# Kernel optimization log

Measured on AMD Instinct MI355X. Metric: run time of the kernel, lower is better.

The kernel has to match this reference:

```python
import jax, jax.numpy as jnp
import numpy as np

N_NODES = 100000
N_EDGES = 1600000
D_IN = 128
D_HID = 64
D_EMB = 64
EDGE_DIM = 2 * D_EMB  # 128
N_CASES = 4
BATCH = 16384
BN_EPS = 1e-5


def gcn_conv(x, src, dst, n, W, b):
    # PyG GCNConv: linear transform, add self-loops, sym-normalized aggregation
    h = x @ W  # [N, out]
    loop = jnp.arange(n, dtype=src.dtype)
    s = jnp.concatenate([src, loop])
    d = jnp.concatenate([dst, loop])
    deg = jax.ops.segment_sum(jnp.ones(s.shape[0], dtype=h.dtype), d, num_segments=n)
    dinv = jnp.where(deg > 0, deg ** -0.5, 0.0)
    norm = dinv[s] * dinv[d]  # [E+N]
    msg = h[s] * norm[:, None]
    return jax.ops.segment_sum(msg, d, num_segments=n) + b


def batchnorm(h, gamma, beta):
    # BatchNorm1d in training mode: biased batch statistics over nodes
    mu = h.mean(0)
    var = jnp.mean((h - mu) ** 2, axis=0)
    return (h - mu) * jax.lax.rsqrt(var + BN_EPS) * gamma + beta


def gcn_net(x, src, dst, n, W1, b1, g, be, W2, b2):
    h = gcn_conv(x, src, dst, n, W1, b1)
    h = jax.nn.relu(batchnorm(h, g, be))
    return gcn_conv(h, src, dst, n, W2, b2)


def setup_inputs() -> dict:
    key = jax.random.key(0)
    ks = jax.random.split(key, 20)
    inp = {
        "x": jax.random.normal(ks[0], (N_NODES, D_IN), dtype=jnp.float32),
        "edge_index": jax.random.randint(ks[1], (2, N_EDGES), 0, N_NODES, dtype=jnp.int32),
        "users_tensor": jax.random.randint(ks[2], (BATCH,), 0, 50000, dtype=jnp.int64) if jax.config.jax_enable_x64 else jax.random.randint(ks[2], (BATCH,), 0, 50000, dtype=jnp.int32),
        "items_tensor": jax.random.randint(ks[3], (BATCH,), 0, N_NODES, dtype=jnp.int32),
    }
    s = 0.05
    # generalized GCN params
    inp["W1g"] = jax.random.normal(ks[4], (D_IN, D_HID), dtype=jnp.float32) * s
    inp["b1g"] = jnp.zeros((D_HID,), jnp.float32)
    inp["g1g"] = jnp.ones((D_HID,), jnp.float32)
    inp["be1g"] = jnp.zeros((D_HID,), jnp.float32)
    inp["W2g"] = jax.random.normal(ks[5], (D_HID, D_EMB), dtype=jnp.float32) * s
    inp["b2g"] = jnp.zeros((D_EMB,), jnp.float32)
    # specific GCN params
    inp["W1s"] = jax.random.normal(ks[6], (D_IN, D_HID), dtype=jnp.float32) * s
    inp["b1s"] = jnp.zeros((D_HID,), jnp.float32)
    inp["g1s"] = jnp.ones((D_HID,), jnp.float32)
    inp["be1s"] = jnp.zeros((D_HID,), jnp.float32)
    inp["W2s"] = jax.random.normal(ks[7], (D_HID, D_EMB), dtype=jnp.float32) * s
    inp["b2s"] = jnp.zeros((D_EMB,), jnp.float32)
    # fusion gate (note: original forward uses hidden1 for BOTH inputs)
    inp["Wf1"] = jax.random.normal(ks[8], (EDGE_DIM, EDGE_DIM), dtype=jnp.float32) * s
    inp["Wsig"] = jax.random.normal(ks[9], (2 * EDGE_DIM, 1), dtype=jnp.float32) * s
    # heads
    inp["Wtc"] = jax.random.normal(ks[10], (EDGE_DIM, N_CASES), dtype=jnp.float32) * s
    inp["btc"] = jnp.zeros((N_CASES,), jnp.float32)
    inp["Wp"] = jax.random.normal(ks[11], (EDGE_DIM, 2), dtype=jnp.float32) * s
    inp["bp"] = jnp.zeros((2,), jnp.float32)
    return inp


def reference(x, edge_index, users_tensor, items_tensor,
              W1g, b1g, g1g, be1g, W2g, b2g,
              W1s, b1s, g1s, be1s, W2s, b2s,
              Wf1, Wsig, Wtc, btc, Wp, bp):
    n = x.shape[0]
    src, dst = edge_index[0], edge_index[1]

    nodes_gen = gcn_net(x, src, dst, n, W1g, b1g, g1g, be1g, W2g, b2g)  # [N, D_EMB]
    nodes_spec = gcn_net(x, src, dst, n, W1s, b1s, g1s, be1s, W2s, b2s)

    gen = jnp.concatenate([nodes_gen[users_tensor], nodes_gen[items_tensor]], axis=1)   # [B, 2E]
    spec = jnp.concatenate([nodes_spec[users_tensor], nodes_spec[items_tensor]], axis=1)

    h1 = jnp.tanh(gen @ Wf1)
    h2 = jnp.tanh(spec @ Wf1)  # original reuses hidden1
    z = jax.nn.sigmoid(jnp.concatenate([h1, h2], axis=1) @ Wsig)  # [B,1]
    fused = z * h1 + (1.0 - z) * h2

    link_output = fused @ Wp + bp
    generalized_output = gen @ Wtc + btc
    return (link_output, generalized_output)
```

## Files before the change

### kernel.cpp

```cpp
#include <hip/hip_runtime.h>
#include <hip/hip_bf16.h>


#define ELL_CAP 64
#define BCAP 8192
#define ACHUNK 5120

typedef __attribute__((ext_vector_type(8))) short short8v;
typedef __attribute__((ext_vector_type(4))) float f32x4;

static __device__ __forceinline__ float wred64(float v) {
#pragma unroll
  for (int m = 32; m; m >>= 1) v += __shfl_xor(v, m, 64);
  return v;
}

static __device__ __forceinline__ unsigned short f2bf(float f) {
  unsigned u = __float_as_uint(f);
  unsigned r = (u + 0x7fffu + ((u >> 16) & 1u)) >> 16;
  return (unsigned short)r;
}
static __device__ __forceinline__ unsigned packbf(float a, float b) {
  return (unsigned)f2bf(a) | ((unsigned)f2bf(b) << 16);
}
static __device__ __forceinline__ float bflo(unsigned u) {
  return __uint_as_float(u << 16);
}
static __device__ __forceinline__ float bfhi(unsigned u) {
  return __uint_as_float(u & 0xffff0000u);
}

__global__ void k_prep(const float* __restrict__ x, unsigned* __restrict__ bff,
                       int* __restrict__ gbump, float* __restrict__ stats,
                       const float* __restrict__ W1g, const float* __restrict__ b1g,
                       const float* __restrict__ W1s, const float* __restrict__ b1s,
                       const float* __restrict__ W2g, const float* __restrict__ b2g,
                       const float* __restrict__ W2s, const float* __restrict__ b2s,
                       const float* __restrict__ Wf1,
                       short* __restrict__ Wb1, short* __restrict__ Wb2,
                       short* __restrict__ WbH, float* __restrict__ bc1,
                       float* __restrict__ bc2, int n, int NB) {
  int idx = blockIdx.x * 256 + threadIdx.x;
  int n16 = n * 16;
  if (idx < n16) {
    const float4* f4 = (const float4*)x;
    float4 a = f4[idx * 2], b = f4[idx * 2 + 1];
    uint4 o;
    o.x = packbf(a.x, a.y);
    o.y = packbf(a.z, a.w);
    o.z = packbf(b.x, b.y);
    o.w = packbf(b.z, b.w);
    ((uint4*)bff)[idx] = o;
  }
  if (idx < 16384) {
    int k = idx >> 7, c = idx & 127;
    int pi = (k >> 3) * 1024 + c * 8 + (k & 7);
    float w1 = (c < 64) ? W1g[k * 64 + c] : W1s[k * 64 + (c - 64)];
    Wb1[pi] = (short)f2bf(w1);
    float w2 = 0.f;
    if (k < 64 && c < 64) w2 = W2g[k * 64 + c];
    else if (k >= 64 && c >= 64) w2 = W2s[(k - 64) * 64 + (c - 64)];
    Wb2[pi] = (short)f2bf(w2);
    WbH[pi] = (short)f2bf(Wf1[k * 128 + c]);
  }
  if (idx < 128) {
    bc1[idx] = (idx < 64) ? b1g[idx] : b1s[idx - 64];
    bc2[idx] = (idx < 64) ? b2g[idx] : b2s[idx - 64];
  }
  if (idx < NB) gbump[idx] = idx * BCAP;
  if (idx < 2048) stats[idx] = 0.f;
}

__global__ __launch_bounds__(256) void k_bucketA(
    const int* __restrict__ src, const int* __restrict__ dst,
    int* __restrict__ gbump, unsigned* __restrict__ ebuf, int E, int NB) {
  __shared__ int hist[512];
  __shared__ int gbase[512];
  int t = threadIdx.x;
  int e0 = blockIdx.x * ACHUNK;
  int m = min(ACHUNK, E - e0);
  for (int b = t; b < NB; b += 256) hist[b] = 0;
  __syncthreads();
  for (int i = t; i < m; i += 256) atomicAdd(&hist[dst[e0 + i] >> 8], 1);
  __syncthreads();
  for (int b = t; b < NB; b += 256) {
    gbase[b] = hist[b] ? atomicAdd(&gbump[b], hist[b]) : 0;
    hist[b] = 0;
  }
  __syncthreads();
  for (int i = t; i < m; i += 256) {
    int d = dst[e0 + i];
    int s = src[e0 + i];
    int b = d >> 8;
    int off = gbase[b] + atomicAdd(&hist[b], 1);
    if (off < (b + 1) * BCAP)
      ebuf[off] = ((unsigned)s << 8) | (unsigned)(d & 255);
  }
}

__global__ __launch_bounds__(256) void k_csrB(
    const unsigned* __restrict__ ebuf, const int* __restrict__ gbump,
    int* __restrict__ cnt, int* __restrict__ col, int n) {
  __shared__ int lbump[256];
  int b = blockIdx.x;
  lbump[threadIdx.x] = 0;
  __syncthreads();
  int base = b * BCAP;
  int m = min(gbump[b] - base, BCAP);
  for (int i = threadIdx.x; i < m; i += 256) {
    unsigned p = ebuf[base + i];
    int dloc = p & 255;
    int slot = atomicAdd(&lbump[dloc], 1);
    if (slot < ELL_CAP)
      col[(b * 256 + dloc) * ELL_CAP + slot] = (int)(p >> 8);
  }
  __syncthreads();
  int node = b * 256 + threadIdx.x;
  if (node < n) cnt[node] = lbump[threadIdx.x];
}

template <bool BN>
__global__ __launch_bounds__(256) void k_agg(
    const unsigned* __restrict__ featb, unsigned* __restrict__ outb,
    const int* __restrict__ cnt, const int* __restrict__ col,
    const float* __restrict__ stats, const float* __restrict__ g1g,
    const float* __restrict__ be1g, const float* __restrict__ g1s,
    const float* __restrict__ be1s, float inv_n, int n) {
  __shared__ float sc_sh[128], sf_sh[128];
  if (BN) {
    int c = threadIdx.x;
    if (c < 128) {
      float s = 0.f, q = 0.f;
#pragma unroll
      for (int k = 0; k < 8; k++) {
        s += stats[k * 256 + c];
        q += stats[k * 256 + 128 + c];
      }
      float mu = s * inv_n;
      float var = q * inv_n - mu * mu;
      float gam = (c < 64) ? g1g[c] : g1s[c - 64];
      float bet = (c < 64) ? be1g[c] : be1s[c - 64];
      float scv = gam * rsqrtf(var + 1e-5f);
      sc_sh[c] = scv;
      sf_sh[c] = bet - mu * scv;
    }
    __syncthreads();
  }
  int node = blockIdx.x * 16 + (threadIdx.x >> 4);
  if (node >= n) return;
  int t = threadIdx.x & 15;
  float sc[8], sf[8];
  if (BN) {
#pragma unroll
    for (int j = 0; j < 8; j++) {
      sc[j] = sc_sh[8 * t + j];
      sf[j] = sf_sh[8 * t + j];
    }
  }
  const uint4* f4 = (const uint4*)featb;
  int cn = cnt[node];
  float di = rsqrtf((float)(cn + 1));
  float acc[8];
  {
    uint4 sv = f4[(size_t)node * 16 + t];
    float f[8] = {bflo(sv.x), bfhi(sv.x), bflo(sv.y), bfhi(sv.y),
                  bflo(sv.z), bfhi(sv.z), bflo(sv.w), bfhi(sv.w)};
#pragma unroll
    for (int j = 0; j < 8; j++) {
      if (BN) f[j] = fmaxf(f[j] * sc[j] + sf[j], 0.f);
      acc[j] = f[j] * di;
    }
  }
  int m = min(cn, ELL_CAP);
  const int4* cl = (const int4*)&col[(size_t)node * ELL_CAP];
  int i = 0;
  for (; i + 4 <= m; i += 4) {
    int4 c4 = cl[i >> 2];
    int ss[4] = {c4.x, c4.y, c4.z, c4.w};
#pragma unroll
    for (int q = 0; q < 4; q++) {
      int s = ss[q];
      float w = rsqrtf((float)(cnt[s] + 1));
      uint4 v = f4[(size_t)s * 16 + t];
      float f[8] = {bflo(v.x), bfhi(v.x), bflo(v.y), bfhi(v.y),
                    bflo(v.z), bfhi(v.z), bflo(v.w), bfhi(v.w)};
#pragma unroll
      for (int j = 0; j < 8; j++) {
        if (BN) f[j] = fmaxf(f[j] * sc[j] + sf[j], 0.f);
        acc[j] += f[j] * w;
      }
    }
  }
  for (; i < m; ++i) {
    int s = col[(size_t)node * ELL_CAP + i];
    float w = rsqrtf((float)(cnt[s] + 1));
    uint4 v = f4[(size_t)s * 16 + t];
    float f[8] = {bflo(v.x), bfhi(v.x), bflo(v.y), bfhi(v.y),
                  bflo(v.z), bfhi(v.z), bflo(v.w), bfhi(v.w)};
#pragma unroll
    for (int j = 0; j < 8; j++) {
      if (BN) f[j] = fmaxf(f[j] * sc[j] + sf[j], 0.f);
      acc[j] += f[j] * w;
    }
  }
  uint4 o;
  o.x = packbf(acc[0] * di, acc[1] * di);
  o.y = packbf(acc[2] * di, acc[3] * di);
  o.z = packbf(acc[4] * di, acc[5] * di);
  o.w = packbf(acc[6] * di, acc[7] * di);
  ((uint4*)outb)[(size_t)node * 16 + t] = o;
}

template <bool CBF16, bool STATS, bool TANH, bool GATHER>
__global__ __launch_bounds__(256) void k_mgemm(
    const unsigned* __restrict__ Abf, const float* __restrict__ nodes,
    const int* __restrict__ users, const int* __restrict__ items,
    const short* __restrict__ Wb, const float* __restrict__ bias,
    void* __restrict__ Cvp, int M, float* __restrict__ stats) {
  __shared__ short Wl[16384];
  __shared__ float shs[128], shq[128];
  {
    const uint4* s4 = (const uint4*)Wb;
    uint4* d4 = (uint4*)Wl;
    for (int i = threadIdx.x; i < 2048; i += 256) d4[i] = s4[i];
  }
  if (STATS && threadIdx.x < 128) { shs[threadIdx.x] = 0.f; shq[threadIdx.x] = 0.f; }
  __syncthreads();
  int lane = threadIdx.x & 63;
  int wv = threadIdx.x >> 6;
  int l15 = lane & 15;
  int l4 = lane >> 4;
  int row = blockIdx.x * 64 + wv * 16 + l15;
  int rc = min(row, M - 1);
  bool valid = row < M;

  short8v afr[4];
  if (GATHER) {
    int fo = blockIdx.y * 64;
    const float* pu = nodes + (size_t)users[rc] * 128 + fo;
    const float* pi = nodes + (size_t)items[rc] * 128 + fo;
#pragma unroll
    for (int ks = 0; ks < 4; ks++) {
      int k = ks * 32 + l4 * 8;
      const float* p = (ks < 2) ? (pu + k) : (pi + (k - 64));
      float4 x0 = *(const float4*)p;
      float4 x1 = *(const float4*)(p + 4);
      union { short s[8]; short8v v; } u;
      u.s[0] = (short)f2bf(x0.x); u.s[1] = (short)f2bf(x0.y);
      u.s[2] = (short)f2bf(x0.z); u.s[3] = (short)f2bf(x0.w);
      u.s[4] = (short)f2bf(x1.x); u.s[5] = (short)f2bf(x1.y);
      u.s[6] = (short)f2bf(x1.z); u.s[7] = (short)f2bf(x1.w);
      afr[ks] = u.v;
    }
  } else {
    const short* Ab = (const short*)Abf + (size_t)rc * 128;
#pragma unroll
    for (int ks = 0; ks < 4; ks++)
      afr[ks] = *(const short8v*)(Ab + ks * 32 + l4 * 8);
  }

  f32x4 acc[8];
#pragma unroll
  for (int nt = 0; nt < 8; nt++) acc[nt] = (f32x4){0.f, 0.f, 0.f, 0.f};
#pragma unroll
  for (int nt = 0; nt < 8; nt++) {
#pragma unroll
    for (int ks = 0; ks < 4; ks++) {
      int kb = ks * 4 + l4;
      short8v w = *(const short8v*)&Wl[kb * 1024 + (nt * 16 + l15) * 8];
      acc[nt] = __builtin_amdgcn_mfma_f32_16x16x32_bf16(w, afr[ks], acc[nt], 0, 0, 0);
    }
  }

#pragma unroll
  for (int nt = 0; nt < 8; nt++) {
    int c0 = nt * 16 + l4 * 4;
    float o[4];
#pragma unroll
    for (int r = 0; r < 4; r++) o[r] = acc[nt][r];
    if (bias) {
      float4 bv = *(const float4*)(bias + c0);
      o[0] += bv.x; o[1] += bv.y; o[2] += bv.z; o[3] += bv.w;
    }
    if (TANH) {
#pragma unroll
      for (int r = 0; r < 4; r++) o[r] = tanhf(o[r]);
    }
    if (STATS) {
      float s[4], q[4];
#pragma unroll
      for (int r = 0; r < 4; r++) {
        s[r] = valid ? o[r] : 0.f;
        q[r] = s[r] * s[r];
      }
#pragma unroll
      for (int m = 1; m < 16; m <<= 1) {
#pragma unroll
        for (int r = 0; r < 4; r++) {
          s[r] += __shfl_xor(s[r], m, 64);
          q[r] += __shfl_xor(q[r], m, 64);
        }
      }
      if (l15 == 0) {
#pragma unroll
        for (int r = 0; r < 4; r++) {
          atomicAdd(&shs[c0 + r], s[r]);
          atomicAdd(&shq[c0 + r], q[r]);
        }
      }
    }
    if (valid) {
      if (CBF16) {
        unsigned* Cb = (unsigned*)Cvp;
        uint2 p;
        p.x = packbf(o[0], o[1]);
        p.y = packbf(o[2], o[3]);
        *(uint2*)&Cb[(size_t)row * 64 + (c0 >> 1)] = p;
      } else {
        float* Cf = (float*)Cvp + (size_t)blockIdx.y * M * 128;
        *(float4*)&Cf[(size_t)row * 128 + c0] = make_float4(o[0], o[1], o[2], o[3]);
      }
    }
  }
  if (STATS) {
    __syncthreads();
    if (threadIdx.x < 128) {
      float* st = stats + (blockIdx.x & 7) * 256;
      atomicAdd(&st[threadIdx.x], shs[threadIdx.x]);
      atomicAdd(&st[128 + threadIdx.x], shq[threadIdx.x]);
    }
  }
}

__global__ void k_head(const float* __restrict__ G1, const float* __restrict__ G2,
                       const float* __restrict__ nodes, const int* __restrict__ users,
                       const int* __restrict__ items, const float* __restrict__ Wsig,
                       const float* __restrict__ Wtc, const float* __restrict__ btc,
                       const float* __restrict__ Wp, const float* __restrict__ bp,
                       float* __restrict__ out, int B) {
  int l = threadIdx.x & 63;
  int wave = (blockIdx.x * 256 + threadIdx.x) >> 6;
  int nw = (gridDim.x * 256) >> 6;
  for (int b = wave; b < B; b += nw) {
    const float* g1 = G1 + (size_t)b * 128;
    const float* g2 = G2 + (size_t)b * 128;
    int u = users[b], it = items[b];
    float h1a = g1[l], h1b = g1[64 + l];
    float h2a = g2[l], h2b = g2[64 + l];
    float ga = nodes[(size_t)u * 128 + l];
    float gb = nodes[(size_t)it * 128 + l];
    float zp = h1a * Wsig[l] + h1b * Wsig[64 + l] + h2a * Wsig[128 + l] + h2b * Wsig[192 + l];
    float z = wred64(zp);
    z = 1.f / (1.f + expf(-z));
    float fa = z * h1a + (1.f - z) * h2a;
    float fb = z * h1b + (1.f - z) * h2b;
    float p0 = wred64(fa * Wp[l * 2] + fb * Wp[(64 + l) * 2]);
    float p1 = wred64(fa * Wp[l * 2 + 1] + fb * Wp[(64 + l) * 2 + 1]);
    float t0 = wred64(ga * Wtc[l * 4] + gb * Wtc[(64 + l) * 4]);
    float t1 = wred64(ga * Wtc[l * 4 + 1] + gb * Wtc[(64 + l) * 4 + 1]);
    float t2 = wred64(ga * Wtc[l * 4 + 2] + gb * Wtc[(64 + l) * 4 + 2]);
    float t3 = wred64(ga * Wtc[l * 4 + 3] + gb * Wtc[(64 + l) * 4 + 3]);
    if (l == 0) {
      out[b * 2] = p0 + bp[0];
      out[b * 2 + 1] = p1 + bp[1];
      float* go = out + 2 * B;
      go[b * 4] = t0 + btc[0];
      go[b * 4 + 1] = t1 + btc[1];
      go[b * 4 + 2] = t2 + btc[2];
      go[b * 4 + 3] = t3 + btc[3];
    }
  }
}

extern "C" void kernel_launch(void* const* d_in, const int* in_sizes, int n_in,
                              void* d_out, int out_size, void* d_ws, size_t ws_size,
                              hipStream_t stream) {
  const float* x = (const float*)d_in[0];
  const int* ei = (const int*)d_in[1];
  const int* users = (const int*)d_in[2];
  const int* items = (const int*)d_in[3];
  const float* W1g = (const float*)d_in[4];
  const float* b1g = (const float*)d_in[5];
  const float* g1g = (const float*)d_in[6];
  const float* be1g = (const float*)d_in[7];
  const float* W2g = (const float*)d_in[8];
  const float* b2g = (const float*)d_in[9];
  const float* W1s = (const float*)d_in[10];
  const float* b1s = (const float*)d_in[11];
  const float* g1s = (const float*)d_in[12];
  const float* be1s = (const float*)d_in[13];
  const float* W2s = (const float*)d_in[14];
  const float* b2s = (const float*)d_in[15];
  const float* Wf1 = (const float*)d_in[16];
  const float* Wsig = (const float*)d_in[17];
  const float* Wtc = (const float*)d_in[18];
  const float* btc = (const float*)d_in[19];
  const float* Wp = (const float*)d_in[20];
  const float* bp = (const float*)d_in[21];

  int n = in_sizes[0] / 128;
  int E = in_sizes[1] / 2;
  int B = in_sizes[2];
  int NB = (n + 255) >> 8;
  const int* srcp = ei;
  const int* dstp = ei + E;
  float* out = (float*)d_out;

  char* w = (char*)d_ws;
  auto alloc = [&](size_t bytes) -> char* {
    char* p = w;
    w += (bytes + 255) & ~(size_t)255;
    return p;
  };
  unsigned* xab = (unsigned*)alloc((size_t)n * 64 * 4);
  float* big1 = (float*)alloc((size_t)n * 128 * 4);
  unsigned* bff = (unsigned*)alloc((size_t)n * 128 * 2);
  int* col = (int*)alloc((size_t)n * ELL_CAP * 4);
  unsigned* ebuf = (unsigned*)alloc((size_t)NB * BCAP * 4);
  int* cnt = (int*)alloc((size_t)n * 4);
  int* gbump = (int*)alloc(512 * 4);
  short* Wb1 = (short*)alloc(16384 * 2);
  short* Wb2 = (short*)alloc(16384 * 2);
  short* WbH = (short*)alloc(16384 * 2);
  float* bc1 = (float*)alloc(512);
  float* bc2 = (float*)alloc(512);
  float* stats = (float*)alloc(2048 * 4);

  k_prep<<<(n * 16 + 255) / 256, 256, 0, stream>>>(
      x, bff, gbump, stats, W1g, b1g, W1s, b1s, W2g, b2g, W2s, b2s, Wf1,
      Wb1, Wb2, WbH, bc1, bc2, n, NB);
  k_bucketA<<<(E + ACHUNK - 1) / ACHUNK, 256, 0, stream>>>(srcp, dstp, gbump, ebuf, E, NB);
  k_csrB<<<NB, 256, 0, stream>>>(ebuf, gbump, cnt, col, n);

  unsigned* hb = (unsigned*)big1;

  k_agg<false><<<(n + 15) / 16, 256, 0, stream>>>(bff, xab, cnt, col, nullptr,
                                                  nullptr, nullptr, nullptr,
                                                  nullptr, 0.f, n);
  k_mgemm<true, true, false, false><<<(n + 63) / 64, 256, 0, stream>>>(
      xab, nullptr, nullptr, nullptr, Wb1, bc1, hb, n, stats);

  k_agg<true><<<(n + 15) / 16, 256, 0, stream>>>(hb, xab, cnt, col, stats, g1g,
                                                 be1g, g1s, be1s, 1.f / (float)n, n);
  k_mgemm<false, false, false, false><<<(n + 63) / 64, 256, 0, stream>>>(
      xab, nullptr, nullptr, nullptr, Wb2, bc2, big1, n, nullptr);

  float* G1 = (float*)bff;
  dim3 gh((B + 63) / 64, 2);
  k_mgemm<false, false, true, true><<<gh, 256, 0, stream>>>(
      nullptr, big1, users, items, WbH, nullptr, G1, B, nullptr);
  float* G2 = G1 + (size_t)B * 128;
  k_head<<<2048, 256, 0, stream>>>(G1, G2, big1, users, items, Wsig, Wtc, btc,
                                   Wp, bp, out, B);
}
```

Before: 259.4 us.

## Sort aggregation nodes by degree and precompute inverse-sqrt degrees

```diff
diff --git a/kernel.cpp b/kernel.cpp
--- a/kernel.cpp
+++ b/kernel.cpp
@@ -32,6 +32,7 @@
 
 __global__ void k_prep(const float* __restrict__ x, unsigned* __restrict__ bff,
                        int* __restrict__ gbump, float* __restrict__ stats,
+                       int* __restrict__ ghist,
                        const float* __restrict__ W1g, const float* __restrict__ b1g,
                        const float* __restrict__ W1s, const float* __restrict__ b1s,
                        const float* __restrict__ W2g, const float* __restrict__ b2g,
@@ -69,6 +70,7 @@
   }
   if (idx < NB) gbump[idx] = idx * BCAP;
   if (idx < 2048) stats[idx] = 0.f;
+  if (idx < 65) ghist[idx] = 0;
 }
 
 __global__ __launch_bounds__(256) void k_bucketA(
@@ -100,7 +102,8 @@
 
 __global__ __launch_bounds__(256) void k_csrB(
     const unsigned* __restrict__ ebuf, const int* __restrict__ gbump,
-    int* __restrict__ cnt, int* __restrict__ col, int n) {
+    int* __restrict__ cnt, float* __restrict__ dinv, int* __restrict__ col,
+    int n) {
   __shared__ int lbump[256];
   int b = blockIdx.x;
   lbump[threadIdx.x] = 0;
@@ -116,13 +119,57 @@
   }
   __syncthreads();
   int node = b * 256 + threadIdx.x;
-  if (node < n) cnt[node] = lbump[threadIdx.x];
+  if (node < n) {
+    int c = lbump[threadIdx.x];
+    cnt[node] = c;
+    dinv[node] = rsqrtf((float)(c + 1));
+  }
+}
+
+__global__ void k_hist(const int* __restrict__ cnt, int* __restrict__ ghist, int n) {
+  __shared__ int h[65];
+  if (threadIdx.x < 65) h[threadIdx.x] = 0;
+  __syncthreads();
+  int i = blockIdx.x * 256 + threadIdx.x;
+  if (i < n) atomicAdd(&h[min(cnt[i], 64)], 1);
+  __syncthreads();
+  if (threadIdx.x < 65 && h[threadIdx.x]) atomicAdd(&ghist[threadIdx.x], h[threadIdx.x]);
+}
+
+__global__ void k_scan65(const int* __restrict__ ghist, int* __restrict__ gbase) {
+  if (threadIdx.x == 0) {
+    int a = 0;
+    for (int b = 64; b >= 0; --b) {
+      gbase[b] = a;
+      a += ghist[b];
+    }
+  }
+}
+
+__global__ void k_scatter(const int* __restrict__ cnt, int* __restrict__ gbase,
+                          int* __restrict__ perm, int n) {
+  __shared__ int h[65];
+  __shared__ int base[65];
+  if (threadIdx.x < 65) h[threadIdx.x] = 0;
+  __syncthreads();
+  int i = blockIdx.x * 256 + threadIdx.x;
+  int b = -1, r = 0;
+  if (i < n) {
+    b = min(cnt[i], 64);
+    r = atomicAdd(&h[b], 1);
+  }
+  __syncthreads();
+  if (threadIdx.x < 65 && h[threadIdx.x])
+    base[threadIdx.x] = atomicAdd(&gbase[threadIdx.x], h[threadIdx.x]);
+  __syncthreads();
+  if (b >= 0) perm[base[b] + r] = i;
 }
 
 template <bool BN>
 __global__ __launch_bounds__(256) void k_agg(
     const unsigned* __restrict__ featb, unsigned* __restrict__ outb,
-    const int* __restrict__ cnt, const int* __restrict__ col,
+    const int* __restrict__ perm, const int* __restrict__ cnt,
+    const float* __restrict__ dinv, const int* __restrict__ col,
     const float* __restrict__ stats, const float* __restrict__ g1g,
     const float* __restrict__ be1g, const float* __restrict__ g1s,
     const float* __restrict__ be1s, float inv_n, int n) {
@@ -146,8 +193,9 @@
     }
     __syncthreads();
   }
-  int node = blockIdx.x * 16 + (threadIdx.x >> 4);
-  if (node >= n) return;
+  int g = blockIdx.x * 16 + (threadIdx.x >> 4);
+  if (g >= n) return;
+  int node = perm[g];
   int t = threadIdx.x & 15;
   float sc[8], sf[8];
   if (BN) {
@@ -158,11 +206,10 @@
     }
   }
   const uint4* f4 = (const uint4*)featb;
-  int cn = cnt[node];
-  float di = rsqrtf((float)(cn + 1));
+  float di = dinv[node];
   float acc[8];
   {
-    uint4 sv = f4[(size_t)node * 16 + t];
+    uint4 sv = f4[node * 16 + t];
     float f[8] = {bflo(sv.x), bfhi(sv.x), bflo(sv.y), bfhi(sv.y),
                   bflo(sv.z), bfhi(sv.z), bflo(sv.w), bfhi(sv.w)};
 #pragma unroll
@@ -171,8 +218,8 @@
       acc[j] = f[j] * di;
     }
   }
-  int m = min(cn, ELL_CAP);
-  const int4* cl = (const int4*)&col[(size_t)node * ELL_CAP];
+  int m = min(cnt[node], ELL_CAP);
+  const int4* cl = (const int4*)&col[node * ELL_CAP];
   int i = 0;
   for (; i + 4 <= m; i += 4) {
     int4 c4 = cl[i >> 2];
@@ -180,8 +227,8 @@
 #pragma unroll
     for (int q = 0; q < 4; q++) {
       int s = ss[q];
-      float w = rsqrtf((float)(cnt[s] + 1));
-      uint4 v = f4[(size_t)s * 16 + t];
+      float w = dinv[s];
+      uint4 v = f4[s * 16 + t];
       float f[8] = {bflo(v.x), bfhi(v.x), bflo(v.y), bfhi(v.y),
                     bflo(v.z), bfhi(v.z), bflo(v.w), bfhi(v.w)};
 #pragma unroll
@@ -192,9 +239,9 @@
     }
   }
   for (; i < m; ++i) {
-    int s = col[(size_t)node * ELL_CAP + i];
-    float w = rsqrtf((float)(cnt[s] + 1));
-    uint4 v = f4[(size_t)s * 16 + t];
+    int s = col[node * ELL_CAP + i];
+    float w = dinv[s];
+    uint4 v = f4[s * 16 + t];
     float f[8] = {bflo(v.x), bfhi(v.x), bflo(v.y), bfhi(v.y),
                   bflo(v.z), bfhi(v.z), bflo(v.w), bfhi(v.w)};
 #pragma unroll
@@ -208,7 +255,7 @@
   o.y = packbf(acc[2] * di, acc[3] * di);
   o.z = packbf(acc[4] * di, acc[5] * di);
   o.w = packbf(acc[6] * di, acc[7] * di);
-  ((uint4*)outb)[(size_t)node * 16 + t] = o;
+  ((uint4*)outb)[node * 16 + t] = o;
 }
 
 template <bool CBF16, bool STATS, bool TANH, bool GATHER>
@@ -418,7 +465,11 @@
   int* col = (int*)alloc((size_t)n * ELL_CAP * 4);
   unsigned* ebuf = (unsigned*)alloc((size_t)NB * BCAP * 4);
   int* cnt = (int*)alloc((size_t)n * 4);
+  float* dinv = (float*)alloc((size_t)n * 4);
+  int* perm = (int*)alloc((size_t)n * 4);
   int* gbump = (int*)alloc(512 * 4);
+  int* ghist = (int*)alloc(128 * 4);
+  int* gbase = (int*)alloc(128 * 4);
   short* Wb1 = (short*)alloc(16384 * 2);
   short* Wb2 = (short*)alloc(16384 * 2);
   short* WbH = (short*)alloc(16384 * 2);
@@ -426,22 +477,29 @@
   float* bc2 = (float*)alloc(512);
   float* stats = (float*)alloc(2048 * 4);
 
+  int nb = (n + 255) / 256;
+
   k_prep<<<(n * 16 + 255) / 256, 256, 0, stream>>>(
-      x, bff, gbump, stats, W1g, b1g, W1s, b1s, W2g, b2g, W2s, b2s, Wf1,
+      x, bff, gbump, stats, ghist, W1g, b1g, W1s, b1s, W2g, b2g, W2s, b2s, Wf1,
       Wb1, Wb2, WbH, bc1, bc2, n, NB);
   k_bucketA<<<(E + ACHUNK - 1) / ACHUNK, 256, 0, stream>>>(srcp, dstp, gbump, ebuf, E, NB);
-  k_csrB<<<NB, 256, 0, stream>>>(ebuf, gbump, cnt, col, n);
+  k_csrB<<<NB, 256, 0, stream>>>(ebuf, gbump, cnt, dinv, col, n);
+
+  k_hist<<<nb, 256, 0, stream>>>(cnt, ghist, n);
+  k_scan65<<<1, 64, 0, stream>>>(ghist, gbase);
+  k_scatter<<<nb, 256, 0, stream>>>(cnt, gbase, perm, n);
 
   unsigned* hb = (unsigned*)big1;
 
-  k_agg<false><<<(n + 15) / 16, 256, 0, stream>>>(bff, xab, cnt, col, nullptr,
+  k_agg<false><<<(n + 15) / 16, 256, 0, stream>>>(bff, xab, perm, cnt, dinv, col,
                                                   nullptr, nullptr, nullptr,
-                                                  nullptr, 0.f, n);
+                                                  nullptr, nullptr, 0.f, n);
   k_mgemm<true, true, false, false><<<(n + 63) / 64, 256, 0, stream>>>(
       xab, nullptr, nullptr, nullptr, Wb1, bc1, hb, n, stats);
 
-  k_agg<true><<<(n + 15) / 16, 256, 0, stream>>>(hb, xab, cnt, col, stats, g1g,
-                                                 be1g, g1s, be1s, 1.f / (float)n, n);
+  k_agg<true><<<(n + 15) / 16, 256, 0, stream>>>(hb, xab, perm, cnt, dinv, col,
+                                                 stats, g1g, be1g, g1s, be1s,
+                                                 1.f / (float)n, n);
   k_mgemm<false, false, false, false><<<(n + 63) / 64, 256, 0, stream>>>(
       xab, nullptr, nullptr, nullptr, Wb2, bc2, big1, n, nullptr);
 
```

Result: slower. 269.2 us (+3.8%).

## Precompute degree norms, batch 8 gathers in aggregation, store final embeddings as bf16

Applied to the files above, without the earlier changes.

```diff
diff --git a/kernel.cpp b/kernel.cpp
--- a/kernel.cpp
+++ b/kernel.cpp
@@ -100,7 +100,8 @@
 
 __global__ __launch_bounds__(256) void k_csrB(
     const unsigned* __restrict__ ebuf, const int* __restrict__ gbump,
-    int* __restrict__ cnt, int* __restrict__ col, int n) {
+    int* __restrict__ cnt, float* __restrict__ dinv, int* __restrict__ col,
+    int n) {
   __shared__ int lbump[256];
   int b = blockIdx.x;
   lbump[threadIdx.x] = 0;
@@ -116,13 +117,18 @@
   }
   __syncthreads();
   int node = b * 256 + threadIdx.x;
-  if (node < n) cnt[node] = lbump[threadIdx.x];
+  if (node < n) {
+    int c = lbump[threadIdx.x];
+    cnt[node] = min(c, ELL_CAP);
+    dinv[node] = rsqrtf((float)(c + 1));
+  }
 }
 
 template <bool BN>
 __global__ __launch_bounds__(256) void k_agg(
     const unsigned* __restrict__ featb, unsigned* __restrict__ outb,
-    const int* __restrict__ cnt, const int* __restrict__ col,
+    const int* __restrict__ cnt, const float* __restrict__ dinv,
+    const int* __restrict__ col,
     const float* __restrict__ stats, const float* __restrict__ g1g,
     const float* __restrict__ be1g, const float* __restrict__ g1s,
     const float* __restrict__ be1s, float inv_n, int n) {
@@ -158,11 +164,10 @@
     }
   }
   const uint4* f4 = (const uint4*)featb;
-  int cn = cnt[node];
-  float di = rsqrtf((float)(cn + 1));
+  float di = dinv[node];
   float acc[8];
   {
-    uint4 sv = f4[(size_t)node * 16 + t];
+    uint4 sv = f4[node * 16 + t];
     float f[8] = {bflo(sv.x), bfhi(sv.x), bflo(sv.y), bfhi(sv.y),
                   bflo(sv.z), bfhi(sv.z), bflo(sv.w), bfhi(sv.w)};
 #pragma unroll
@@ -171,17 +176,41 @@
       acc[j] = f[j] * di;
     }
   }
-  int m = min(cn, ELL_CAP);
-  const int4* cl = (const int4*)&col[(size_t)node * ELL_CAP];
+  int m = cnt[node];
+  const int4* cl = (const int4*)&col[node * ELL_CAP];
   int i = 0;
+  for (; i + 8 <= m; i += 8) {
+    int4 c0 = cl[i >> 2];
+    int4 c1 = cl[(i >> 2) + 1];
+    int ss[8] = {c0.x, c0.y, c0.z, c0.w, c1.x, c1.y, c1.z, c1.w};
+    float ww[8];
+    uint4 vv[8];
+#pragma unroll
+    for (int q = 0; q < 8; q++) {
+      ww[q] = dinv[ss[q]];
+      vv[q] = f4[ss[q] * 16 + t];
+    }
+#pragma unroll
+    for (int q = 0; q < 8; q++) {
+      float w = ww[q];
+      uint4 v = vv[q];
+      float f[8] = {bflo(v.x), bfhi(v.x), bflo(v.y), bfhi(v.y),
+                    bflo(v.z), bfhi(v.z), bflo(v.w), bfhi(v.w)};
+#pragma unroll
+      for (int j = 0; j < 8; j++) {
+        if (BN) f[j] = fmaxf(f[j] * sc[j] + sf[j], 0.f);
+        acc[j] += f[j] * w;
+      }
+    }
+  }
   for (; i + 4 <= m; i += 4) {
     int4 c4 = cl[i >> 2];
     int ss[4] = {c4.x, c4.y, c4.z, c4.w};
 #pragma unroll
     for (int q = 0; q < 4; q++) {
       int s = ss[q];
-      float w = rsqrtf((float)(cnt[s] + 1));
-      uint4 v = f4[(size_t)s * 16 + t];
+      float w = dinv[s];
+      uint4 v = f4[s * 16 + t];
       float f[8] = {bflo(v.x), bfhi(v.x), bflo(v.y), bfhi(v.y),
                     bflo(v.z), bfhi(v.z), bflo(v.w), bfhi(v.w)};
 #pragma unroll
@@ -192,9 +221,9 @@
     }
   }
   for (; i < m; ++i) {
-    int s = col[(size_t)node * ELL_CAP + i];
-    float w = rsqrtf((float)(cnt[s] + 1));
-    uint4 v = f4[(size_t)s * 16 + t];
+    int s = col[node * ELL_CAP + i];
+    float w = dinv[s];
+    uint4 v = f4[s * 16 + t];
     float f[8] = {bflo(v.x), bfhi(v.x), bflo(v.y), bfhi(v.y),
                   bflo(v.z), bfhi(v.z), bflo(v.w), bfhi(v.w)};
 #pragma unroll
@@ -208,12 +237,12 @@
   o.y = packbf(acc[2] * di, acc[3] * di);
   o.z = packbf(acc[4] * di, acc[5] * di);
   o.w = packbf(acc[6] * di, acc[7] * di);
-  ((uint4*)outb)[(size_t)node * 16 + t] = o;
+  ((uint4*)outb)[node * 16 + t] = o;
 }
 
 template <bool CBF16, bool STATS, bool TANH, bool GATHER>
 __global__ __launch_bounds__(256) void k_mgemm(
-    const unsigned* __restrict__ Abf, const float* __restrict__ nodes,
+    const unsigned* __restrict__ Abf, const unsigned short* __restrict__ nodesb,
     const int* __restrict__ users, const int* __restrict__ items,
     const short* __restrict__ Wb, const float* __restrict__ bias,
     void* __restrict__ Cvp, int M, float* __restrict__ stats) {
@@ -237,20 +266,13 @@
   short8v afr[4];
   if (GATHER) {
     int fo = blockIdx.y * 64;
-    const float* pu = nodes + (size_t)users[rc] * 128 + fo;
-    const float* pi = nodes + (size_t)items[rc] * 128 + fo;
+    const short* pu = (const short*)nodesb + users[rc] * 128 + fo;
+    const short* pi = (const short*)nodesb + items[rc] * 128 + fo;
 #pragma unroll
     for (int ks = 0; ks < 4; ks++) {
       int k = ks * 32 + l4 * 8;
-      const float* p = (ks < 2) ? (pu + k) : (pi + (k - 64));
-      float4 x0 = *(const float4*)p;
-      float4 x1 = *(const float4*)(p + 4);
-      union { short s[8]; short8v v; } u;
-      u.s[0] = (short)f2bf(x0.x); u.s[1] = (short)f2bf(x0.y);
-      u.s[2] = (short)f2bf(x0.z); u.s[3] = (short)f2bf(x0.w);
-      u.s[4] = (short)f2bf(x1.x); u.s[5] = (short)f2bf(x1.y);
-      u.s[6] = (short)f2bf(x1.z); u.s[7] = (short)f2bf(x1.w);
-      afr[ks] = u.v;
+      const short* p = (ks < 2) ? (pu + k) : (pi + (k - 64));
+      afr[ks] = *(const short8v*)p;
     }
   } else {
     const short* Ab = (const short*)Abf + (size_t)rc * 128;
@@ -333,7 +355,8 @@
 }
 
 __global__ void k_head(const float* __restrict__ G1, const float* __restrict__ G2,
-                       const float* __restrict__ nodes, const int* __restrict__ users,
+                       const unsigned short* __restrict__ nodesb,
+                       const int* __restrict__ users,
                        const int* __restrict__ items, const float* __restrict__ Wsig,
                        const float* __restrict__ Wtc, const float* __restrict__ btc,
                        const float* __restrict__ Wp, const float* __restrict__ bp,
@@ -347,8 +370,8 @@
     int u = users[b], it = items[b];
     float h1a = g1[l], h1b = g1[64 + l];
     float h2a = g2[l], h2b = g2[64 + l];
-    float ga = nodes[(size_t)u * 128 + l];
-    float gb = nodes[(size_t)it * 128 + l];
+    float ga = __uint_as_float((unsigned)nodesb[u * 128 + l] << 16);
+    float gb = __uint_as_float((unsigned)nodesb[it * 128 + l] << 16);
     float zp = h1a * Wsig[l] + h1b * Wsig[64 + l] + h2a * Wsig[128 + l] + h2b * Wsig[192 + l];
     float z = wred64(zp);
     z = 1.f / (1.f + expf(-z));
@@ -418,6 +441,7 @@
   int* col = (int*)alloc((size_t)n * ELL_CAP * 4);
   unsigned* ebuf = (unsigned*)alloc((size_t)NB * BCAP * 4);
   int* cnt = (int*)alloc((size_t)n * 4);
+  float* dinv = (float*)alloc((size_t)n * 4);
   int* gbump = (int*)alloc(512 * 4);
   short* Wb1 = (short*)alloc(16384 * 2);
   short* Wb2 = (short*)alloc(16384 * 2);
@@ -430,26 +454,28 @@
       x, bff, gbump, stats, W1g, b1g, W1s, b1s, W2g, b2g, W2s, b2s, Wf1,
       Wb1, Wb2, WbH, bc1, bc2, n, NB);
   k_bucketA<<<(E + ACHUNK - 1) / ACHUNK, 256, 0, stream>>>(srcp, dstp, gbump, ebuf, E, NB);
-  k_csrB<<<NB, 256, 0, stream>>>(ebuf, gbump, cnt, col, n);
+  k_csrB<<<NB, 256, 0, stream>>>(ebuf, gbump, cnt, dinv, col, n);
 
   unsigned* hb = (unsigned*)big1;
-
-  k_agg<false><<<(n + 15) / 16, 256, 0, stream>>>(bff, xab, cnt, col, nullptr,
+  unsigned short* nodesb = (unsigned short*)big1;
+
+  k_agg<false><<<(n + 15) / 16, 256, 0, stream>>>(bff, xab, cnt, dinv, col,
                                                   nullptr, nullptr, nullptr,
-                                                  nullptr, 0.f, n);
+                                                  nullptr, nullptr, 0.f, n);
   k_mgemm<true, true, false, false><<<(n + 63) / 64, 256, 0, stream>>>(
       xab, nullptr, nullptr, nullptr, Wb1, bc1, hb, n, stats);
 
-  k_agg<true><<<(n + 15) / 16, 256, 0, stream>>>(hb, xab, cnt, col, stats, g1g,
-                                                 be1g, g1s, be1s, 1.f / (float)n, n);
-  k_mgemm<false, false, false, false><<<(n + 63) / 64, 256, 0, stream>>>(
-      xab, nullptr, nullptr, nullptr, Wb2, bc2, big1, n, nullptr);
+  k_agg<true><<<(n + 15) / 16, 256, 0, stream>>>(hb, xab, cnt, dinv, col,
+                                                 stats, g1g, be1g, g1s, be1s,
+                                                 1.f / (float)n, n);
+  k_mgemm<true, false, false, false><<<(n + 63) / 64, 256, 0, stream>>>(
+      xab, nullptr, nullptr, nullptr, Wb2, bc2, nodesb, n, nullptr);
 
   float* G1 = (float*)bff;
   dim3 gh((B + 63) / 64, 2);
   k_mgemm<false, false, true, true><<<gh, 256, 0, stream>>>(
-      nullptr, big1, users, items, WbH, nullptr, G1, B, nullptr);
+      nullptr, nodesb, users, items, WbH, nullptr, G1, B, nullptr);
   float* G2 = G1 + (size_t)B * 128;
-  k_head<<<2048, 256, 0, stream>>>(G1, G2, big1, users, items, Wsig, Wtc, btc,
+  k_head<<<2048, 256, 0, stream>>>(G1, G2, nodesb, users, items, Wsig, Wtc, btc,
                                    Wp, bp, out, B);
 }
```

Measured after the change: 275.8 us. +6.3%, slower.
